# Kernel tuning notes

Hardware: AMD Instinct MI355X
Metric: run time of the kernel (lower is better)

The kernel has to match this reference:

```python
import jax, jax.numpy as jnp
import numpy as np
from jax import lax

R = 1          # guided filter radius
EPS = 1e-05    # regularizer


def _box_filter(x, r):
    # Separable moving-average, VALID padding (matches Keras DepthwiseConv2D default).
    # Original applies filter_y (k,1) first, then filter_x (1,k).
    k = 2 * r + 1
    c = x.shape[-1]
    ky = jnp.full((k, 1, 1, c), 1.0 / k, x.dtype)  # HWIO depthwise kernel
    kx = jnp.full((1, k, 1, c), 1.0 / k, x.dtype)
    dn = lax.conv_dimension_numbers(x.shape, ky.shape, ('NHWC', 'HWIO', 'NHWC'))
    x = lax.conv_general_dilated(x, ky, (1, 1), 'VALID', dimension_numbers=dn,
                                 feature_group_count=c)
    x = lax.conv_general_dilated(x, kx, (1, 1), 'VALID', dimension_numbers=dn,
                                 feature_group_count=c)
    return x


def setup_inputs() -> dict:
    key = jax.random.key(0)
    k1, k2, k3 = jax.random.split(key, 3)
    lr_x = jax.random.normal(k1, (2, 270, 480, 4), jnp.float32)
    lr_y = jax.random.normal(k2, (2, 270, 480, 4), jnp.float32)
    hr_x = jax.random.normal(k3, (2, 1080, 1920, 4), jnp.float32)
    return {"lr_x": lr_x, "lr_y": lr_y, "hr_x": hr_x}


def reference(lr_x, lr_y, hr_x):
    mean_x = _box_filter(lr_x, R)                              # [B, H-2r, W-2r, C]
    mean_y = _box_filter(lr_y, R)
    cov_xy = _box_filter(lr_x * lr_y, R) - mean_x * mean_y
    var_x = _box_filter(lr_x * lr_x, R) - mean_x * mean_x
    A = cov_xy / (var_x + EPS)
    b = mean_y - A * mean_x
    B, H, W, C = hr_x.shape
    mean_A = jax.image.resize(A, (B, H, W, C), method='bilinear', antialias=False)
    mean_b = jax.image.resize(b, (B, H, W, C), method='bilinear', antialias=False)
    return mean_A * hr_x + mean_b
```

## Files before the change

### kernel.cpp

```cpp
#include <hip/hip_runtime.h>


namespace {

constexpr int LR_H = 270, LR_W = 480;
constexpr int A_H  = 268, A_W  = 478;
constexpr int HR_H = 1080, HR_W = 1920;
constexpr int BATCH = 2;
constexpr float EPS_F = 1e-5f;

constexpr int TILE_W = 240;
constexpr int NTILES = HR_W / TILE_W;
constexpr int ROWS   = 5;
constexpr int ROWGRP = HR_H / ROWS;
constexpr int VCOLS  = 64;
constexpr int ACOLS  = 62;
constexpr int RSETS  = 3;

__device__ __forceinline__ float4 f4add(float4 a, float4 b) {
    return make_float4(a.x + b.x, a.y + b.y, a.z + b.z, a.w + b.w);
}
__device__ __forceinline__ float4 f4sub(float4 a, float4 b) {
    return make_float4(a.x - b.x, a.y - b.y, a.z - b.z, a.w - b.w);
}
__device__ __forceinline__ float4 f4mul(float4 a, float4 b) {
    return make_float4(a.x * b.x, a.y * b.y, a.z * b.z, a.w * b.w);
}
__device__ __forceinline__ float4 f4scale(float4 a, float s) {
    return make_float4(a.x * s, a.y * s, a.z * s, a.w * s);
}
__device__ __forceinline__ float4 f4fma(float4 a, float4 b, float4 c) {
    return make_float4(fmaf(a.x, b.x, c.x), fmaf(a.y, b.y, c.y),
                       fmaf(a.z, b.z, c.z), fmaf(a.w, b.w, c.w));
}
__device__ __forceinline__ float4 f4lerp(float4 a, float4 b, float t) {
    return make_float4(fmaf(t, b.x - a.x, a.x), fmaf(t, b.y - a.y, a.y),
                       fmaf(t, b.z - a.z, a.z), fmaf(t, b.w - a.w, a.w));
}
__device__ __forceinline__ float4 f4axpy(float s, float4 v, float4 acc) {
    return make_float4(fmaf(s, v.x, acc.x), fmaf(s, v.y, acc.y),
                       fmaf(s, v.z, acc.z), fmaf(s, v.w, acc.w));
}
__device__ __forceinline__ float4 f4rcp(float4 a) {
    return make_float4(__builtin_amdgcn_rcpf(a.x), __builtin_amdgcn_rcpf(a.y),
                       __builtin_amdgcn_rcpf(a.z), __builtin_amdgcn_rcpf(a.w));
}

}

__global__ __launch_bounds__(256) void
fgf_fused5(const float4* __restrict__ lr_x,
           const float4* __restrict__ lr_y,
           const float4* __restrict__ hr_x,
           float4* __restrict__ out) {
    __shared__ float4 vs[RSETS][4][VCOLS];
    __shared__ float4 sA4[RSETS][ACOLS];
    __shared__ float4 sB4[RSETS][ACOLS];

    int bid  = blockIdx.x;
    int tile = bid & (NTILES - 1);
    int g    = bid >> 3;
    int rg   = g % ROWGRP;
    int b    = g / ROWGRP;
    int tid  = threadIdx.x;

    constexpr float sh_scale = (float)A_H / (float)HR_H;
    constexpr float sw_scale = (float)A_W / (float)HR_W;

    int hbase = rg * ROWS;
    int R0 = (int)floorf((hbase + 0.5f) * sh_scale - 0.5f);

    int w_start = tile * TILE_W;
    int c0 = (int)floorf((w_start + 0.5f) * sw_scale - 0.5f);

    int w = w_start + tid;
    bool valid = (tid < TILE_W);
    size_t hr_row0 = ((size_t)b * HR_H + hbase) * (size_t)HR_W + w;
    float4 xr[ROWS];
#pragma unroll
    for (int j = 0; j < ROWS; ++j) {
        xr[j] = valid ? hr_x[hr_row0 + (size_t)j * HR_W]
                      : make_float4(0.f, 0.f, 0.f, 0.f);
    }

    if (tid < RSETS * VCOLS) {
        int rs = tid >> 6;
        int cs = tid & 63;
        int ar = min(max(R0 + rs, 0), A_H - 1);
        int col = min(max(c0 + cs, 0), LR_W - 1);
        const float4* px = lr_x + ((size_t)b * LR_H + ar) * LR_W + col;
        const float4* py = lr_y + ((size_t)b * LR_H + ar) * LR_W + col;
        float4 sx  = make_float4(0.f, 0.f, 0.f, 0.f);
        float4 sy  = make_float4(0.f, 0.f, 0.f, 0.f);
        float4 sxy = make_float4(0.f, 0.f, 0.f, 0.f);
        float4 sxx = make_float4(0.f, 0.f, 0.f, 0.f);
#pragma unroll
        for (int dy = 0; dy < 3; ++dy) {
            float4 x = px[(size_t)dy * LR_W];
            float4 y = py[(size_t)dy * LR_W];
            sx  = f4add(sx, x);
            sy  = f4add(sy, y);
            sxy = f4fma(x, y, sxy);
            sxx = f4fma(x, x, sxx);
        }
        vs[rs][0][cs] = sx;
        vs[rs][1][cs] = sy;
        vs[rs][2][cs] = sxy;
        vs[rs][3][cs] = sxx;
    }
    __syncthreads();

    constexpr float inv9 = 1.0f / 9.0f;
    {
        int rs = tid >> 6;
        int sl = tid & 63;
        if (rs < RSETS && sl < ACOLS) {
            int a  = min(max(c0 + sl, 0), A_W - 1);
            int bs = a - c0;
            float4 hx  = f4add(f4add(vs[rs][0][bs], vs[rs][0][bs + 1]), vs[rs][0][bs + 2]);
            float4 hy  = f4add(f4add(vs[rs][1][bs], vs[rs][1][bs + 1]), vs[rs][1][bs + 2]);
            float4 hxy = f4add(f4add(vs[rs][2][bs], vs[rs][2][bs + 1]), vs[rs][2][bs + 2]);
            float4 hxx = f4add(f4add(vs[rs][3][bs], vs[rs][3][bs + 1]), vs[rs][3][bs + 2]);
            float4 mx  = f4scale(hx, inv9);
            float4 my  = f4scale(hy, inv9);
            float4 cov = f4sub(f4scale(hxy, inv9), f4mul(mx, my));
            float4 var = f4sub(f4scale(hxx, inv9), f4mul(mx, mx));
            float4 A = f4mul(cov, f4rcp(make_float4(var.x + EPS_F, var.y + EPS_F,
                                                    var.z + EPS_F, var.w + EPS_F)));
            float4 bb = f4sub(my, f4mul(A, mx));
            sA4[rs][sl] = A;
            sB4[rs][sl] = bb;
        }
    }
    __syncthreads();

    if (valid) {
        float sw = (w + 0.5f) * sw_scale - 0.5f;
        float fw = floorf(sw);
        float tw = sw - fw;
        int wi = min((int)fw - c0, ACOLS - 2);

        float4 hA0 = f4lerp(sA4[0][wi], sA4[0][wi + 1], tw);
        float4 hB0 = f4lerp(sB4[0][wi], sB4[0][wi + 1], tw);
        float4 hA1 = f4lerp(sA4[1][wi], sA4[1][wi + 1], tw);
        float4 hB1 = f4lerp(sB4[1][wi], sB4[1][wi + 1], tw);
        float4 hA2 = f4lerp(sA4[2][wi], sA4[2][wi + 1], tw);
        float4 hB2 = f4lerp(sB4[2][wi], sB4[2][wi + 1], tw);

#pragma unroll
        for (int j = 0; j < ROWS; ++j) {
            float shj = (hbase + j + 0.5f) * sh_scale - 0.5f;
            float t = shj - (float)R0;
            float w0 = fmaxf(1.f - t, 0.f);
            float w1 = 1.f - fabsf(t - 1.f);
            float w2 = fmaxf(t - 1.f, 0.f);

            float4 aI = f4axpy(w2, hA2, f4axpy(w1, hA1, f4scale(hA0, w0)));
            float4 bI = f4axpy(w2, hB2, f4axpy(w1, hB1, f4scale(hB0, w0)));

            out[hr_row0 + (size_t)j * HR_W] = f4fma(aI, xr[j], bI);
        }
    }
}

extern "C" void kernel_launch(void* const* d_in, const int* in_sizes, int n_in,
                              void* d_out, int out_size, void* d_ws, size_t ws_size,
                              hipStream_t stream) {
    const float4* lr_x = (const float4*)d_in[0];
    const float4* lr_y = (const float4*)d_in[1];
    const float4* hr_x = (const float4*)d_in[2];
    float4* out = (float4*)d_out;

    constexpr int nblocks = BATCH * ROWGRP * NTILES;
    fgf_fused5<<<nblocks, 256, 0, stream>>>(lr_x, lr_y, hr_x, out);
}
```

Before: 26.50 us.

## Convert fused guided filter to persistent blocks with atomic work stealing

Replaces the one-block-per-tile grid with a fixed 2048-block persistent grid. Each block repeatedly pulls a tile index from a global atomic counter in workspace, which a hipMemsetAsync zeroes before launch. The aim is to balance load and cut block launch and tail overhead across the roughly 3456 tiles. In exchange it adds a memset operation, one atomic per tile, an extra barrier per iteration, and it serializes the per-tile phases inside each block.

```diff
diff --git a/kernel.cpp b/kernel.cpp
--- a/kernel.cpp
+++ b/kernel.cpp
@@ -13,9 +13,12 @@
 constexpr int NTILES = HR_W / TILE_W;
 constexpr int ROWS   = 5;
 constexpr int ROWGRP = HR_H / ROWS;
+constexpr int NTASK  = BATCH * ROWGRP * NTILES;
 constexpr int VCOLS  = 64;
 constexpr int ACOLS  = 62;
 constexpr int RSETS  = 3;
+
+constexpr int NBLOCKS = 2048;
 
 __device__ __forceinline__ float4 f4add(float4 a, float4 b) {
     return make_float4(a.x + b.x, a.y + b.y, a.z + b.z, a.w + b.w);
@@ -49,78 +52,87 @@
 }
 
 __global__ __launch_bounds__(256) void
-fgf_fused5(const float4* __restrict__ lr_x,
-           const float4* __restrict__ lr_y,
-           const float4* __restrict__ hr_x,
-           float4* __restrict__ out) {
+fgf_steal(const float4* __restrict__ lr_x,
+          const float4* __restrict__ lr_y,
+          const float4* __restrict__ hr_x,
+          float4* __restrict__ out,
+          unsigned* __restrict__ ctr) {
     __shared__ float4 vs[RSETS][4][VCOLS];
     __shared__ float4 sA4[RSETS][ACOLS];
     __shared__ float4 sB4[RSETS][ACOLS];
+    __shared__ unsigned sTask;
 
-    int bid  = blockIdx.x;
-    int tile = bid & (NTILES - 1);
-    int g    = bid >> 3;
-    int rg   = g % ROWGRP;
-    int b    = g / ROWGRP;
-    int tid  = threadIdx.x;
+    int tid = threadIdx.x;
 
     constexpr float sh_scale = (float)A_H / (float)HR_H;
     constexpr float sw_scale = (float)A_W / (float)HR_W;
+    constexpr float inv9 = 1.0f / 9.0f;
 
-    int hbase = rg * ROWS;
-    int R0 = (int)floorf((hbase + 0.5f) * sh_scale - 0.5f);
+    int rsA = min(tid, RSETS * VCOLS - 1) >> 6;
+    int csA = tid & 63;
+    bool aAct = (tid < RSETS * VCOLS);
+    int rsB = tid >> 6;
+    int slB = tid & 63;
+    bool bAct = (rsB < RSETS) && (slB < ACOLS);
+    bool valid = (tid < TILE_W);
 
-    int w_start = tile * TILE_W;
-    int c0 = (int)floorf((w_start + 0.5f) * sw_scale - 0.5f);
+    for (;;) {
+        if (tid == 0) sTask = atomicAdd(ctr, 1u);
+        __syncthreads();
+        unsigned task = sTask;
+        if (task >= (unsigned)NTASK) break;
 
-    int w = w_start + tid;
-    bool valid = (tid < TILE_W);
-    size_t hr_row0 = ((size_t)b * HR_H + hbase) * (size_t)HR_W + w;
-    float4 xr[ROWS];
+        int tile = task & (NTILES - 1);
+        int g    = task >> 3;
+        int rg   = g % ROWGRP;
+        int b    = g / ROWGRP;
+
+        int hbase = rg * ROWS;
+        int R0 = (int)floorf((hbase + 0.5f) * sh_scale - 0.5f);
+        int w_start = tile * TILE_W;
+        int c0 = (int)floorf((w_start + 0.5f) * sw_scale - 0.5f);
+
+        int w = w_start + tid;
+        size_t hr_row0 = ((size_t)b * HR_H + hbase) * (size_t)HR_W + w;
+        float4 xr[ROWS];
 #pragma unroll
-    for (int j = 0; j < ROWS; ++j) {
-        xr[j] = valid ? hr_x[hr_row0 + (size_t)j * HR_W]
-                      : make_float4(0.f, 0.f, 0.f, 0.f);
-    }
+        for (int j = 0; j < ROWS; ++j) {
+            xr[j] = valid ? hr_x[hr_row0 + (size_t)j * HR_W]
+                          : make_float4(0.f, 0.f, 0.f, 0.f);
+        }
 
-    if (tid < RSETS * VCOLS) {
-        int rs = tid >> 6;
-        int cs = tid & 63;
-        int ar = min(max(R0 + rs, 0), A_H - 1);
-        int col = min(max(c0 + cs, 0), LR_W - 1);
-        const float4* px = lr_x + ((size_t)b * LR_H + ar) * LR_W + col;
-        const float4* py = lr_y + ((size_t)b * LR_H + ar) * LR_W + col;
-        float4 sx  = make_float4(0.f, 0.f, 0.f, 0.f);
-        float4 sy  = make_float4(0.f, 0.f, 0.f, 0.f);
-        float4 sxy = make_float4(0.f, 0.f, 0.f, 0.f);
-        float4 sxx = make_float4(0.f, 0.f, 0.f, 0.f);
+        if (aAct) {
+            int ar = min(max(R0 + rsA, 0), A_H - 1);
+            int col = min(max(c0 + csA, 0), LR_W - 1);
+            const float4* px = lr_x + ((size_t)b * LR_H + ar) * LR_W + col;
+            const float4* py = lr_y + ((size_t)b * LR_H + ar) * LR_W + col;
+            float4 sx  = make_float4(0.f, 0.f, 0.f, 0.f);
+            float4 sy  = make_float4(0.f, 0.f, 0.f, 0.f);
+            float4 sxy = make_float4(0.f, 0.f, 0.f, 0.f);
+            float4 sxx = make_float4(0.f, 0.f, 0.f, 0.f);
 #pragma unroll
-        for (int dy = 0; dy < 3; ++dy) {
-            float4 x = px[(size_t)dy * LR_W];
-            float4 y = py[(size_t)dy * LR_W];
-            sx  = f4add(sx, x);
-            sy  = f4add(sy, y);
-            sxy = f4fma(x, y, sxy);
-            sxx = f4fma(x, x, sxx);
+            for (int dy = 0; dy < 3; ++dy) {
+                float4 x = px[(size_t)dy * LR_W];
+                float4 y = py[(size_t)dy * LR_W];
+                sx  = f4add(sx, x);
+                sy  = f4add(sy, y);
+                sxy = f4fma(x, y, sxy);
+                sxx = f4fma(x, x, sxx);
+            }
+            vs[rsA][0][csA] = sx;
+            vs[rsA][1][csA] = sy;
+            vs[rsA][2][csA] = sxy;
+            vs[rsA][3][csA] = sxx;
         }
-        vs[rs][0][cs] = sx;
-        vs[rs][1][cs] = sy;
-        vs[rs][2][cs] = sxy;
-        vs[rs][3][cs] = sxx;
-    }
-    __syncthreads();
+        __syncthreads();
 
-    constexpr float inv9 = 1.0f / 9.0f;
-    {
-        int rs = tid >> 6;
-        int sl = tid & 63;
-        if (rs < RSETS && sl < ACOLS) {
-            int a  = min(max(c0 + sl, 0), A_W - 1);
+        if (bAct) {
+            int a  = min(max(c0 + slB, 0), A_W - 1);
             int bs = a - c0;
-            float4 hx  = f4add(f4add(vs[rs][0][bs], vs[rs][0][bs + 1]), vs[rs][0][bs + 2]);
-            float4 hy  = f4add(f4add(vs[rs][1][bs], vs[rs][1][bs + 1]), vs[rs][1][bs + 2]);
-            float4 hxy = f4add(f4add(vs[rs][2][bs], vs[rs][2][bs + 1]), vs[rs][2][bs + 2]);
-            float4 hxx = f4add(f4add(vs[rs][3][bs], vs[rs][3][bs + 1]), vs[rs][3][bs + 2]);
+            float4 hx  = f4add(f4add(vs[rsB][0][bs], vs[rsB][0][bs + 1]), vs[rsB][0][bs + 2]);
+            float4 hy  = f4add(f4add(vs[rsB][1][bs], vs[rsB][1][bs + 1]), vs[rsB][1][bs + 2]);
+            float4 hxy = f4add(f4add(vs[rsB][2][bs], vs[rsB][2][bs + 1]), vs[rsB][2][bs + 2]);
+            float4 hxx = f4add(f4add(vs[rsB][3][bs], vs[rsB][3][bs + 1]), vs[rsB][3][bs + 2]);
             float4 mx  = f4scale(hx, inv9);
             float4 my  = f4scale(hy, inv9);
             float4 cov = f4sub(f4scale(hxy, inv9), f4mul(mx, my));
@@ -128,37 +140,37 @@
             float4 A = f4mul(cov, f4rcp(make_float4(var.x + EPS_F, var.y + EPS_F,
                                                     var.z + EPS_F, var.w + EPS_F)));
             float4 bb = f4sub(my, f4mul(A, mx));
-            sA4[rs][sl] = A;
-            sB4[rs][sl] = bb;
+            sA4[rsB][slB] = A;
+            sB4[rsB][slB] = bb;
         }
-    }
-    __syncthreads();
+        __syncthreads();
 
-    if (valid) {
-        float sw = (w + 0.5f) * sw_scale - 0.5f;
-        float fw = floorf(sw);
-        float tw = sw - fw;
-        int wi = min((int)fw - c0, ACOLS - 2);
+        if (valid) {
+            float swf = (w + 0.5f) * sw_scale - 0.5f;
+            float fw = floorf(swf);
+            float tw = swf - fw;
+            int wi = min((int)fw - c0, ACOLS - 2);
 
-        float4 hA0 = f4lerp(sA4[0][wi], sA4[0][wi + 1], tw);
-        float4 hB0 = f4lerp(sB4[0][wi], sB4[0][wi + 1], tw);
-        float4 hA1 = f4lerp(sA4[1][wi], sA4[1][wi + 1], tw);
-        float4 hB1 = f4lerp(sB4[1][wi], sB4[1][wi + 1], tw);
-        float4 hA2 = f4lerp(sA4[2][wi], sA4[2][wi + 1], tw);
-        float4 hB2 = f4lerp(sB4[2][wi], sB4[2][wi + 1], tw);
+            float4 hA0 = f4lerp(sA4[0][wi], sA4[0][wi + 1], tw);
+            float4 hB0 = f4lerp(sB4[0][wi], sB4[0][wi + 1], tw);
+            float4 hA1 = f4lerp(sA4[1][wi], sA4[1][wi + 1], tw);
+            float4 hB1 = f4lerp(sB4[1][wi], sB4[1][wi + 1], tw);
+            float4 hA2 = f4lerp(sA4[2][wi], sA4[2][wi + 1], tw);
+            float4 hB2 = f4lerp(sB4[2][wi], sB4[2][wi + 1], tw);
 
 #pragma unroll
-        for (int j = 0; j < ROWS; ++j) {
-            float shj = (hbase + j + 0.5f) * sh_scale - 0.5f;
-            float t = shj - (float)R0;
-            float w0 = fmaxf(1.f - t, 0.f);
-            float w1 = 1.f - fabsf(t - 1.f);
-            float w2 = fmaxf(t - 1.f, 0.f);
+            for (int j = 0; j < ROWS; ++j) {
+                float shj = (hbase + j + 0.5f) * sh_scale - 0.5f;
+                float t = shj - (float)R0;
+                float w0 = fmaxf(1.f - t, 0.f);
+                float w1 = 1.f - fabsf(t - 1.f);
+                float w2 = fmaxf(t - 1.f, 0.f);
 
-            float4 aI = f4axpy(w2, hA2, f4axpy(w1, hA1, f4scale(hA0, w0)));
-            float4 bI = f4axpy(w2, hB2, f4axpy(w1, hB1, f4scale(hB0, w0)));
+                float4 aI = f4axpy(w2, hA2, f4axpy(w1, hA1, f4scale(hA0, w0)));
+                float4 bI = f4axpy(w2, hB2, f4axpy(w1, hB1, f4scale(hB0, w0)));
 
-            out[hr_row0 + (size_t)j * HR_W] = f4fma(aI, xr[j], bI);
+                out[hr_row0 + (size_t)j * HR_W] = f4fma(aI, xr[j], bI);
+            }
         }
     }
 }
@@ -171,6 +183,7 @@
     const float4* hr_x = (const float4*)d_in[2];
     float4* out = (float4*)d_out;
 
-    constexpr int nblocks = BATCH * ROWGRP * NTILES;
-    fgf_fused5<<<nblocks, 256, 0, stream>>>(lr_x, lr_y, hr_x, out);
+    hipMemsetAsync(d_ws, 0, sizeof(unsigned), stream);
+    fgf_steal<<<NBLOCKS, 256, 0, stream>>>(lr_x, lr_y, hr_x, out,
+                                           (unsigned*)d_ws);
 }
```

New measurement: 79.71 us. +200.8%, slower.
